# Kernel tuning notes

Hardware: AMD Instinct MI355X
Metric: run time of the kernel (lower is better)

Reference implementation:

```python
import jax, jax.numpy as jnp
import numpy as np

N, C, T, V, D = 64, 64, 256, 25, 64
BN_EPS = 1e-5


def _make_shift(v, ch, sign):
    idx = np.empty(v * ch, dtype=np.int64)
    for i in range(v):
        for j in range(ch):
            idx[i * ch + j] = (i * ch + j + sign * j * ch) % (ch * v)
    return jnp.asarray(idx, dtype=jnp.int32)


def setup_inputs() -> dict:
    key = jax.random.key(0)
    ks = jax.random.split(key, 8)
    return {
        "x0": jax.random.normal(ks[0], (N, C, T, V), dtype=jnp.float32),
        "fc1_w": jax.random.normal(ks[1], (C // 4, C), dtype=jnp.float32) * (1.0 / np.sqrt(C)),
        "fc1_b": jnp.zeros((C // 4,), dtype=jnp.float32),
        "fc2_w": jax.random.normal(ks[2], (4, C // 4), dtype=jnp.float32) * (1.0 / np.sqrt(C // 4)),
        "fc2_b": jnp.zeros((4,), dtype=jnp.float32),
        "Linear_weight": jax.random.normal(ks[3], (4, C, D), dtype=jnp.float32) * np.sqrt(1.0 / D),
        "Linear_bias": jax.random.normal(ks[4], (4, D), dtype=jnp.float32) * 0.02,
        "Feature_Mask": jax.random.normal(ks[5], (1, V, C), dtype=jnp.float32) * 0.1,
        "bn_gamma": 1.0 + 0.05 * jax.random.normal(ks[6], (V * D,), dtype=jnp.float32),
        "bn_beta": 0.05 * jax.random.normal(ks[7], (V * D,), dtype=jnp.float32),
        "shift_in": _make_shift(V, C, +1),
        "shift_out": _make_shift(V, D, -1),
        "epoch": 100,
    }


def reference(x0, fc1_w, fc1_b, fc2_w, fc2_b, Linear_weight, Linear_bias,
              Feature_Mask, bn_gamma, bn_beta, shift_in, shift_out, epoch):
    n, c, t, v = x0.shape
    d = Linear_weight.shape[-1]

    # DY_SEModule gate: global avg pool -> 1x1 convs -> tempered softmax over 4
    pooled = x0.mean(axis=(2, 3))                       # [n, c]
    h = jax.nn.relu(pooled @ fc1_w.T + fc1_b)           # [n, c//4]
    logits = h @ fc2_w.T + fc2_b                        # [n, 4]
    tao = (-(30.0 - 1.0) / 60.0 * epoch + 30.0) if epoch < 60 else 1.0
    gate = jax.nn.softmax(logits / tao, axis=1)         # [n, 4]

    # per-sample fused weights / bias
    W_fuse = jnp.einsum('kcd,nk->ncd', Linear_weight, gate)   # [n, c, d]
    b_fuse = jnp.einsum('kc,nk->nc', Linear_bias, gate)       # [n, d]

    # shift-in gather over flattened (v*c) channel axis
    x = x0.transpose(0, 2, 3, 1).reshape(n * t, v * c)  # [n*t, v*c]
    x = x[:, shift_in].reshape(n * t, v, c)
    x = x * (jnp.tanh(Feature_Mask) + 1.0)              # learnable feature mask
    x = x.reshape(n, t, v, c)

    # per-sample dynamic linear + bias
    x = jnp.einsum('ntvc,ncd->ntvd', x, W_fuse) + b_fuse[:, None, None, :]

    # shift-out gather
    x = x.reshape(n * t, v * d)[:, shift_out]           # [n*t, v*d]

    # BatchNorm1d (training mode: batch statistics over n*t)
    mean = x.mean(axis=0)
    var = jnp.var(x, axis=0)
    x = (x - mean) * jax.lax.rsqrt(var + BN_EPS) * bn_gamma + bn_beta

    x = x.reshape(n, t, v, d).transpose(0, 3, 1, 2)     # [n, d, t, v]
    return jax.nn.relu(x + x0)                          # identity residual (c == d)
```

## Files before the change

kernel.cpp:

```cpp
#include <hip/hip_runtime.h>
#include <hip/hip_bf16.h>
#include <math.h>

#define NN 64
#define CC 64
#define TT 256
#define VV 25
#define DD 64
#define BN_EPS 1e-5f

typedef short bf16x8 __attribute__((ext_vector_type(8)));
typedef float f32x4 __attribute__((ext_vector_type(4)));

#define WS_POOLED 0
#define WS_GATE   4096
#define WS_BFUSE  4352
#define WS_MASK   8448
#define WS_ABP    10048
#define WS_PART2  13248
#define WS_WTB    218048
#define WS_YB     349120

static __device__ __forceinline__ unsigned short f2bf(float x) {
    __hip_bfloat16 h = __float2bfloat16(x);
    return *(unsigned short*)&h;
}
static __device__ __forceinline__ unsigned short f2bf_fast(float x) {
    return (unsigned short)((__float_as_uint(x) + 0x8000u) >> 16);
}
static __device__ __forceinline__ float bf2f(unsigned short u) {
    return __uint_as_float(((unsigned)u) << 16);
}

__global__ __launch_bounds__(256) void k_pool(const float* __restrict__ x0,
                                              float* __restrict__ pooled) {
    __shared__ float red[256];
    const int bid = blockIdx.x;
    const float4* p = (const float4*)(x0 + (size_t)bid * (TT * VV));
    float4 xv[7];
#pragma unroll
    for (int it = 0; it < 7; it++) {
        const int k = threadIdx.x + it * 256;
        if (k < 1600) xv[it] = p[k];
    }
    float s = 0.f;
#pragma unroll
    for (int it = 0; it < 7; it++) {
        const int k = threadIdx.x + it * 256;
        if (k < 1600) s += xv[it].x + xv[it].y + xv[it].z + xv[it].w;
    }
    red[threadIdx.x] = s;
    __syncthreads();
    for (int off = 128; off > 0; off >>= 1) {
        if (threadIdx.x < off) red[threadIdx.x] += red[threadIdx.x + off];
        __syncthreads();
    }
    if (threadIdx.x == 0) pooled[bid] = red[0] * (1.f / (TT * VV));
}

__global__ __launch_bounds__(256) void k_gate(const float* __restrict__ fc1_w,
                                              const float* __restrict__ fc1_b,
                                              const float* __restrict__ fc2_w,
                                              const float* __restrict__ fc2_b,
                                              const float* __restrict__ lin_b,
                                              const float* __restrict__ fmask,
                                              const int* __restrict__ epoch_p,
                                              float* ws) {
    const int tid = threadIdx.x;
    float* pooled = ws + WS_POOLED;
    float* gate   = ws + WS_GATE;
    float* bfuse  = ws + WS_BFUSE;

    for (int f = tid; f < VV * CC; f += 256) ws[WS_MASK + f] = tanhf(fmask[f]) + 1.0f;

    if (tid < 64) {
        const int n = tid;
        const float* po = pooled + n * 64;
        float h[16];
        for (int q = 0; q < 16; q++) {
            float z = fc1_b[q];
            for (int j = 0; j < 64; j++) z = fmaf(fc1_w[q * 64 + j], po[j], z);
            h[q] = fmaxf(z, 0.f);
        }
        float lg[4];
        for (int k = 0; k < 4; k++) {
            float z = fc2_b[k];
            for (int q = 0; q < 16; q++) z = fmaf(fc2_w[k * 16 + q], h[q], z);
            lg[k] = z;
        }
        const int ep = epoch_p[0];
        const float tao = (ep < 60) ? (-(29.0f / 60.0f) * (float)ep + 30.0f) : 1.0f;
        float mx = -1e30f;
        for (int k = 0; k < 4; k++) { lg[k] /= tao; mx = fmaxf(mx, lg[k]); }
        float se = 0.f;
        for (int k = 0; k < 4; k++) { lg[k] = expf(lg[k] - mx); se += lg[k]; }
        const float inv = 1.f / se;
        for (int k = 0; k < 4; k++) gate[n * 4 + k] = lg[k] * inv;
    }
    __syncthreads();
    for (int f = tid; f < 4096; f += 256) {
        const int n = f >> 6, d = f & 63;
        float s = 0.f;
        for (int k = 0; k < 4; k++) s = fmaf(lin_b[k * 64 + d], gate[n * 4 + k], s);
        bfuse[f] = s;
    }
}

__global__ __launch_bounds__(256) void k_wfuse(const float* __restrict__ lw, float* ws) {
    __shared__ float tile[64 * 65];
    const float* gate = ws + WS_GATE;
    unsigned short* wtb = (unsigned short*)(ws + WS_WTB);
    const int n = blockIdx.x;
    float g[4];
    for (int k = 0; k < 4; k++) g[k] = gate[n * 4 + k];
    for (int f = threadIdx.x; f < 4096; f += 256) {
        const int c = f >> 6, d = f & 63;
        float v = g[0] * lw[f] + g[1] * lw[4096 + f] + g[2] * lw[8192 + f] + g[3] * lw[12288 + f];
        tile[d * 65 + c] = v;
    }
    __syncthreads();
    for (int f = threadIdx.x; f < 4096; f += 256) {
        const int d = f >> 6, c = f & 63;
        wtb[n * 4096 + f] = f2bf(tile[d * 65 + c]);
    }
}

__global__ __launch_bounds__(256) void k_maing(const float* __restrict__ x0,
                                               const unsigned short* __restrict__ wtb,
                                               const float* __restrict__ ws,
                                               float* __restrict__ wsmut,
                                               float2* __restrict__ scr) {
    __shared__ __align__(16) char pool[35456];
    float* maskL = (float*)pool;
    unsigned short (*Xm)[72] = (unsigned short(*)[72])(pool + 6528);
    const int n = blockIdx.y, tb = blockIdx.x;
    const int tid = threadIdx.x;
    const int wv = tid >> 6, lane = tid & 63;
    const int lrow = lane & 15, lgrp = lane >> 4;
    const int dcol = wv * 16 + lrow;
    unsigned short* outw = (unsigned short*)(pool + 22656) + wv * 1600;

    for (int f = tid; f < 1600; f += 256)
        maskL[(f >> 6) * 65 + (f & 63)] = ws[WS_MASK + f];
    for (int f = tid; f < 864; f += 256) ((unsigned short*)Xm)[7200 + f] = 0;
    const bf16x8 w0 = *(const bf16x8*)(wtb + n * 4096 + dcol * 64 + 8 * lgrp);
    const bf16x8 w1 = *(const bf16x8*)(wtb + n * 4096 + dcol * 64 + 32 + 8 * lgrp);
    const float bfv = ws[WS_BFUSE + n * 64 + dcol];
    __syncthreads();

    float s1r[7][4], s2r[7][4];
#pragma unroll
    for (int m = 0; m < 7; m++)
#pragma unroll
        for (int r = 0; r < 4; r++) { s1r[m][r] = 0.f; s2r[m][r] = 0.f; }

    const size_t nbase = (size_t)n * (CC * TT * VV);
    unsigned short* yg = (unsigned short*)(wsmut + WS_YB) + (size_t)n * 64 * 6400;

    for (int ck = 0; ck < 4; ck++) {
        const int gcol0 = tb * 400 + ck * 100;
        if (ck) __syncthreads();

        float4 xv[7];
#pragma unroll
        for (int it = 0; it < 7; it++) {
            const int l4 = tid + it * 256;
            if (l4 < 1600) {
                const int j = l4 / 25, q = l4 - j * 25;
                xv[it] = *(const float4*)(x0 + nbase + j * 6400 + gcol0 + q * 4);
            }
        }
#pragma unroll
        for (int it = 0; it < 7; it++) {
            const int l4 = tid + it * 256;
            if (l4 < 1600) {
                const int j = l4 / 25, q = l4 - j * 25;
                int jm = j; if (jm >= 50) jm -= 50; else if (jm >= 25) jm -= 25;
                const float xe[4] = {xv[it].x, xv[it].y, xv[it].z, xv[it].w};
#pragma unroll
                for (int e = 0; e < 4; e++) {
                    const int r = q * 4 + e;
                    const int trel = (r >= 75) ? 3 : (r >= 50) ? 2 : (r >= 25) ? 1 : 0;
                    const int p = r - trel * 25;
                    int i = p - jm; if (i < 0) i += 25;
                    Xm[trel * 25 + i][j] = f2bf_fast(xe[e] * maskL[i * 65 + j]);
                }
            }
        }
        __syncthreads();

#pragma unroll
        for (int m = 0; m < 7; m++) {
            const bf16x8 a0 = *(const bf16x8*)&Xm[m * 16 + lrow][8 * lgrp];
            const bf16x8 a1 = *(const bf16x8*)&Xm[m * 16 + lrow][32 + 8 * lgrp];
            f32x4 a = {bfv, bfv, bfv, bfv};
            a = __builtin_amdgcn_mfma_f32_16x16x32_bf16(a0, w0, a, 0, 0, 0);
            a = __builtin_amdgcn_mfma_f32_16x16x32_bf16(a1, w1, a, 0, 0, 0);
#pragma unroll
            for (int r = 0; r < 4; r++) {
                const int row = m * 16 + 4 * lgrp + r;
                if (row < 100) {
                    const unsigned short us = f2bf_fast(a[r]);
                    const float yf = bf2f(us);
                    s1r[m][r] += yf;
                    s2r[m][r] = fmaf(yf, yf, s2r[m][r]);
                    outw[lrow * 100 + row] = us;
                }
            }
        }
#pragma unroll
        for (int it = 0; it < 7; it++) {
            const int l = lane + it * 64;
            if (l < 400) {
                const int dloc = l / 25, q = l - dloc * 25;
                const uint2 u = *(const uint2*)(outw + dloc * 100 + 4 * q);
                *(uint2*)(yg + (size_t)(wv * 16 + dloc) * 6400 + gcol0 + 4 * q) = u;
            }
        }
    }

    __syncthreads();
    float* s1l = (float*)pool;
    float* s2l = s1l + 1650;
    for (int f = tid; f < 3300; f += 256) s1l[f] = 0.f;
    __syncthreads();
#pragma unroll
    for (int m = 0; m < 7; m++) {
#pragma unroll
        for (int r = 0; r < 4; r++) {
            const int row = m * 16 + 4 * lgrp + r;
            if (row < 100) {
                int vv = row;
                if (vv >= 75) vv -= 75; else if (vv >= 50) vv -= 50; else if (vv >= 25) vv -= 25;
                __hip_atomic_fetch_add(&s1l[vv * 66 + dcol], s1r[m][r],
                                       __ATOMIC_RELAXED, __HIP_MEMORY_SCOPE_WORKGROUP);
                __hip_atomic_fetch_add(&s2l[vv * 66 + dcol], s2r[m][r],
                                       __ATOMIC_RELAXED, __HIP_MEMORY_SCOPE_WORKGROUP);
            }
        }
    }
    __syncthreads();
    float2* part = scr + (size_t)(n * 16 + tb) * 1600;
    for (int f = tid; f < 1600; f += 256) {
        float2 p;
        p.x = s1l[(f >> 6) * 66 + (f & 63)];
        p.y = s2l[(f >> 6) * 66 + (f & 63)];
        part[f] = p;
    }
}

__global__ __launch_bounds__(256) void k_fred(const float2* __restrict__ scr, float* ws) {
    const int f = blockIdx.x * 256 + threadIdx.x;
    if (f >= VV * DD) return;
    const int slice = blockIdx.y;
    const float2* part = scr + (size_t)slice * 32 * 1600;
    float a0 = 0.f, a1 = 0.f, a2 = 0.f, a3 = 0.f;
    float c0 = 0.f, c1 = 0.f, c2 = 0.f, c3 = 0.f;
#pragma unroll 4
    for (int b = 0; b < 32; b += 4) {
        const float2 p0 = part[(size_t)(b + 0) * 1600 + f];
        const float2 p1 = part[(size_t)(b + 1) * 1600 + f];
        const float2 p2 = part[(size_t)(b + 2) * 1600 + f];
        const float2 p3 = part[(size_t)(b + 3) * 1600 + f];
        a0 += p0.x; c0 += p0.y;
        a1 += p1.x; c1 += p1.y;
        a2 += p2.x; c2 += p2.y;
        a3 += p3.x; c3 += p3.y;
    }
    float2 o;
    o.x = (a0 + a1) + (a2 + a3);
    o.y = (c0 + c1) + (c2 + c3);
    ((float2*)(ws + WS_PART2))[(size_t)slice * 1600 + f] = o;
}

__global__ __launch_bounds__(256) void k_finalize(const float* __restrict__ gamma,
                                                  const float* __restrict__ beta,
                                                  float* ws) {
    const int f = blockIdx.x * 256 + threadIdx.x;
    if (f >= VV * DD) return;
    const int v = f >> 6, d = f & 63;
    const int vi = (v - d + 175) % 25;
    const int fin = vi * 64 + d;

    const float2* part2 = (const float2*)(ws + WS_PART2);
    float a0 = 0.f, a1 = 0.f, a2 = 0.f, a3 = 0.f;
    float c0 = 0.f, c1 = 0.f, c2 = 0.f, c3 = 0.f;
#pragma unroll 4
    for (int b = 0; b < 32; b += 4) {
        const float2 p0 = part2[(size_t)(b + 0) * 1600 + fin];
        const float2 p1 = part2[(size_t)(b + 1) * 1600 + fin];
        const float2 p2 = part2[(size_t)(b + 2) * 1600 + fin];
        const float2 p3 = part2[(size_t)(b + 3) * 1600 + fin];
        a0 += p0.x; c0 += p0.y;
        a1 += p1.x; c1 += p1.y;
        a2 += p2.x; c2 += p2.y;
        a3 += p3.x; c3 += p3.y;
    }
    const float s1 = (a0 + a1) + (a2 + a3);
    const float s2 = (c0 + c1) + (c2 + c3);

    const float mean = s1 * (1.f / (NN * TT));
    float var = s2 * (1.f / (NN * TT)) - mean * mean;
    var = fmaxf(var, 0.f);
    const float rs = rsqrtf(var + BN_EPS);
    const float a = gamma[f] * rs;
    const float b = beta[f] - mean * a;
    ((unsigned*)ws)[WS_ABP + f] = (unsigned)f2bf(a) | (((unsigned)f2bf(b)) << 16);
}

__global__ __launch_bounds__(256) void k_bn(const float* __restrict__ x0,
                                            const float* __restrict__ ws,
                                            float* __restrict__ out) {
    __shared__ __align__(16) unsigned short ybL[6400];
    __shared__ float aL[25], bL[25];
    const int d = blockIdx.x, n = blockIdx.y;
    const int tid = threadIdx.x;
    const size_t pbase = (size_t)(n * 64 + d) * 6400;
    const unsigned short* yb = (const unsigned short*)(ws + WS_YB);

    for (int l = tid; l < 800; l += 256)
        *(uint4*)&ybL[l * 8] = *(const uint4*)(yb + pbase + l * 8);
    if (tid < 25) {
        const unsigned u = ((const unsigned*)ws)[WS_ABP + tid * 64 + d];
        aL[tid] = __uint_as_float(u << 16);
        bL[tid] = __uint_as_float(u & 0xffff0000u);
    }
    __syncthreads();

    const int sh = d % 25;
    for (int l4 = tid; l4 < 1600; l4 += 256) {
        const int e0 = 4 * l4;
        const float4 xv = *(const float4*)(x0 + pbase + e0);
        int t = e0 / 25;
        int vo = e0 - 25 * t;
        float o[4];
        const float xe[4] = {xv.x, xv.y, xv.z, xv.w};
#pragma unroll
        for (int k = 0; k < 4; k++) {
            int vs = vo - sh; if (vs < 0) vs += 25;
            const float y = bf2f(ybL[t * 25 + vs]);
            o[k] = fmaxf(fmaf(aL[vo], y, bL[vo]) + xe[k], 0.f);
            vo++; if (vo >= 25) { vo = 0; t++; }
        }
        float4 ov = {o[0], o[1], o[2], o[3]};
        *(float4*)(out + pbase + e0) = ov;
    }
}

extern "C" void kernel_launch(void* const* d_in, const int* in_sizes, int n_in,
                              void* d_out, int out_size, void* d_ws, size_t ws_size,
                              hipStream_t stream) {
    const float* x0    = (const float*)d_in[0];
    const float* fc1_w = (const float*)d_in[1];
    const float* fc1_b = (const float*)d_in[2];
    const float* fc2_w = (const float*)d_in[3];
    const float* fc2_b = (const float*)d_in[4];
    const float* lw    = (const float*)d_in[5];
    const float* lb    = (const float*)d_in[6];
    const float* fmask = (const float*)d_in[7];
    const float* gamma = (const float*)d_in[8];
    const float* beta  = (const float*)d_in[9];
    const int* epoch   = (const int*)d_in[12];
    float* ws  = (float*)d_ws;
    float* out = (float*)d_out;
    float2* scr = (float2*)d_out;
    const unsigned short* wtb = (const unsigned short*)(ws + WS_WTB);

    k_pool<<<NN * CC, 256, 0, stream>>>(x0, ws + WS_POOLED);
    k_gate<<<1, 256, 0, stream>>>(fc1_w, fc1_b, fc2_w, fc2_b, lb, fmask, epoch, ws);
    k_wfuse<<<NN, 256, 0, stream>>>(lw, ws);
    k_maing<<<dim3(16, 64), 256, 0, stream>>>(x0, wtb, ws, ws, scr);
    k_fred<<<dim3(7, 32), 256, 0, stream>>>(scr, ws);
    k_finalize<<<7, 256, 0, stream>>>(gamma, beta, ws);
    k_bn<<<dim3(64, 64), 256, 0, stream>>>(x0, ws, out);
}
```

Baseline: 203.5 us.

## Store intermediate Y as [t*v][d] and write MFMA results directly to global

The operand order of the MFMA is swapped so each lane holds four consecutive d outputs for one row. The bf16 result is then written straight to global memory in a row-major [n][t*v][d] layout, replacing the LDS staging buffer and its separate copy-out loop. This shrinks k_maing's shared memory and removes a staging pass. k_bn is reorganised so each block handles 100 columns across all 64 d, reading the contiguous y tile and the full BN scale/shift table into LDS. The trade-off is less coalesced 8-byte scattered stores from the MFMA stage and strided LDS reads in k_bn.

After: 224.9 us. 1.11x slower.

```diff
diff --git a/kernel.cpp b/kernel.cpp
--- a/kernel.cpp
+++ b/kernel.cpp
@@ -130,7 +130,7 @@
                                                const float* __restrict__ ws,
                                                float* __restrict__ wsmut,
                                                float2* __restrict__ scr) {
-    __shared__ __align__(16) char pool[35456];
+    __shared__ __align__(16) char pool[22656];
     float* maskL = (float*)pool;
     unsigned short (*Xm)[72] = (unsigned short(*)[72])(pool + 6528);
     const int n = blockIdx.y, tb = blockIdx.x;
@@ -138,14 +138,14 @@
     const int wv = tid >> 6, lane = tid & 63;
     const int lrow = lane & 15, lgrp = lane >> 4;
     const int dcol = wv * 16 + lrow;
-    unsigned short* outw = (unsigned short*)(pool + 22656) + wv * 1600;
+    const int dout = wv * 16 + 4 * lgrp;
 
     for (int f = tid; f < 1600; f += 256)
         maskL[(f >> 6) * 65 + (f & 63)] = ws[WS_MASK + f];
     for (int f = tid; f < 864; f += 256) ((unsigned short*)Xm)[7200 + f] = 0;
     const bf16x8 w0 = *(const bf16x8*)(wtb + n * 4096 + dcol * 64 + 8 * lgrp);
     const bf16x8 w1 = *(const bf16x8*)(wtb + n * 4096 + dcol * 64 + 32 + 8 * lgrp);
-    const float bfv = ws[WS_BFUSE + n * 64 + dcol];
+    const float4 b4 = *(const float4*)&ws[WS_BFUSE + n * 64 + dout];
     __syncthreads();
 
     float s1r[7][4], s2r[7][4];
@@ -155,7 +155,7 @@
         for (int r = 0; r < 4; r++) { s1r[m][r] = 0.f; s2r[m][r] = 0.f; }
 
     const size_t nbase = (size_t)n * (CC * TT * VV);
-    unsigned short* yg = (unsigned short*)(wsmut + WS_YB) + (size_t)n * 64 * 6400;
+    unsigned short* yg = (unsigned short*)(wsmut + WS_YB) + (size_t)n * 6400 * 64;
 
     for (int ck = 0; ck < 4; ck++) {
         const int gcol0 = tb * 400 + ck * 100;
@@ -193,28 +193,23 @@
         for (int m = 0; m < 7; m++) {
             const bf16x8 a0 = *(const bf16x8*)&Xm[m * 16 + lrow][8 * lgrp];
             const bf16x8 a1 = *(const bf16x8*)&Xm[m * 16 + lrow][32 + 8 * lgrp];
-            f32x4 a = {bfv, bfv, bfv, bfv};
-            a = __builtin_amdgcn_mfma_f32_16x16x32_bf16(a0, w0, a, 0, 0, 0);
-            a = __builtin_amdgcn_mfma_f32_16x16x32_bf16(a1, w1, a, 0, 0, 0);
-#pragma unroll
-            for (int r = 0; r < 4; r++) {
-                const int row = m * 16 + 4 * lgrp + r;
-                if (row < 100) {
-                    const unsigned short us = f2bf_fast(a[r]);
-                    const float yf = bf2f(us);
+            f32x4 a = {b4.x, b4.y, b4.z, b4.w};
+            a = __builtin_amdgcn_mfma_f32_16x16x32_bf16(w0, a0, a, 0, 0, 0);
+            a = __builtin_amdgcn_mfma_f32_16x16x32_bf16(w1, a1, a, 0, 0, 0);
+            const int row = m * 16 + lrow;
+            if (row < 100) {
+                unsigned short us[4];
+#pragma unroll
+                for (int r = 0; r < 4; r++) {
+                    us[r] = f2bf_fast(a[r]);
+                    const float yf = bf2f(us[r]);
                     s1r[m][r] += yf;
                     s2r[m][r] = fmaf(yf, yf, s2r[m][r]);
-                    outw[lrow * 100 + row] = us;
                 }
-            }
-        }
-#pragma unroll
-        for (int it = 0; it < 7; it++) {
-            const int l = lane + it * 64;
-            if (l < 400) {
-                const int dloc = l / 25, q = l - dloc * 25;
-                const uint2 u = *(const uint2*)(outw + dloc * 100 + 4 * q);
-                *(uint2*)(yg + (size_t)(wv * 16 + dloc) * 6400 + gcol0 + 4 * q) = u;
+                uint2 u;
+                u.x = (unsigned)us[0] | ((unsigned)us[1] << 16);
+                u.y = (unsigned)us[2] | ((unsigned)us[3] << 16);
+                *(uint2*)(yg + (size_t)(gcol0 + row) * 64 + dout) = u;
             }
         }
     }
@@ -226,15 +221,15 @@
     __syncthreads();
 #pragma unroll
     for (int m = 0; m < 7; m++) {
-#pragma unroll
-        for (int r = 0; r < 4; r++) {
-            const int row = m * 16 + 4 * lgrp + r;
-            if (row < 100) {
-                int vv = row;
-                if (vv >= 75) vv -= 75; else if (vv >= 50) vv -= 50; else if (vv >= 25) vv -= 25;
-                __hip_atomic_fetch_add(&s1l[vv * 66 + dcol], s1r[m][r],
+        const int row = m * 16 + lrow;
+        if (row < 100) {
+            int vv = row;
+            if (vv >= 75) vv -= 75; else if (vv >= 50) vv -= 50; else if (vv >= 25) vv -= 25;
+#pragma unroll
+            for (int r = 0; r < 4; r++) {
+                __hip_atomic_fetch_add(&s1l[vv * 66 + dout + r], s1r[m][r],
                                        __ATOMIC_RELAXED, __HIP_MEMORY_SCOPE_WORKGROUP);
-                __hip_atomic_fetch_add(&s2l[vv * 66 + dcol], s2r[m][r],
+                __hip_atomic_fetch_add(&s2l[vv * 66 + dout + r], s2r[m][r],
                                        __ATOMIC_RELAXED, __HIP_MEMORY_SCOPE_WORKGROUP);
             }
         }
@@ -311,39 +306,44 @@
 __global__ __launch_bounds__(256) void k_bn(const float* __restrict__ x0,
                                             const float* __restrict__ ws,
                                             float* __restrict__ out) {
-    __shared__ __align__(16) unsigned short ybL[6400];
-    __shared__ float aL[25], bL[25];
-    const int d = blockIdx.x, n = blockIdx.y;
+    __shared__ __align__(16) unsigned short yL[100 * 68];
+    __shared__ unsigned ABl[25 * 68];
+    const int tcb = blockIdx.x, n = blockIdx.y;
     const int tid = threadIdx.x;
-    const size_t pbase = (size_t)(n * 64 + d) * 6400;
-    const unsigned short* yb = (const unsigned short*)(ws + WS_YB);
-
-    for (int l = tid; l < 800; l += 256)
-        *(uint4*)&ybL[l * 8] = *(const uint4*)(yb + pbase + l * 8);
-    if (tid < 25) {
-        const unsigned u = ((const unsigned*)ws)[WS_ABP + tid * 64 + d];
-        aL[tid] = __uint_as_float(u << 16);
-        bL[tid] = __uint_as_float(u & 0xffff0000u);
-    }
-    __syncthreads();
-
-    const int sh = d % 25;
+    const int col0 = tcb * 100;
+    const unsigned short* yg = (const unsigned short*)(ws + WS_YB) + ((size_t)n * 6400 + col0) * 64;
+
+    for (int g = tid; g < 1600; g += 256) {
+        const uint2 u = *(const uint2*)(yg + g * 4);
+        *(uint2*)&yL[(g >> 4) * 68 + (g & 15) * 4] = u;
+    }
+    const unsigned* abp = (const unsigned*)(ws + WS_ABP);
+    for (int f = tid; f < 1600; f += 256)
+        ABl[(f >> 6) * 68 + (f & 63)] = abp[f];
+    __syncthreads();
+
+    const size_t pbase = (size_t)n * (CC * TT * VV);
     for (int l4 = tid; l4 < 1600; l4 += 256) {
-        const int e0 = 4 * l4;
-        const float4 xv = *(const float4*)(x0 + pbase + e0);
-        int t = e0 / 25;
-        int vo = e0 - 25 * t;
+        const int dd = l4 / 25, q = l4 - dd * 25;
+        const int c0 = 4 * q;
+        const float4 xv = *(const float4*)(x0 + pbase + dd * 6400 + col0 + c0);
+        const int sh = dd - ((dd >= 50) ? 50 : (dd >= 25) ? 25 : 0);
         float o[4];
         const float xe[4] = {xv.x, xv.y, xv.z, xv.w};
 #pragma unroll
         for (int k = 0; k < 4; k++) {
+            const int col = c0 + k;
+            const int tl = (col >= 75) ? 3 : (col >= 50) ? 2 : (col >= 25) ? 1 : 0;
+            const int vo = col - tl * 25;
             int vs = vo - sh; if (vs < 0) vs += 25;
-            const float y = bf2f(ybL[t * 25 + vs]);
-            o[k] = fmaxf(fmaf(aL[vo], y, bL[vo]) + xe[k], 0.f);
-            vo++; if (vo >= 25) { vo = 0; t++; }
+            const unsigned u = ABl[vo * 68 + dd];
+            const float a_ = __uint_as_float(u << 16);
+            const float b_ = __uint_as_float(u & 0xffff0000u);
+            const float y = bf2f(yL[(tl * 25 + vs) * 68 + dd]);
+            o[k] = fmaxf(fmaf(a_, y, b_) + xe[k], 0.f);
         }
         float4 ov = {o[0], o[1], o[2], o[3]};
-        *(float4*)(out + pbase + e0) = ov;
+        *(float4*)(out + pbase + dd * 6400 + col0 + c0) = ov;
     }
 }
 
```
